# Optimization experiments

Measured on AMD Instinct MI355X. Metric: run time of the kernel, lower is better.

## Reference

```python
import jax, jax.numpy as jnp
import numpy as np

SIMOTA_Q = 10
W_CLS, W_GEOM, W_IOU, W_DIST, W_THETA = 4.0, 5.0, 2.0, 1.0, 2.0
INVALID = -100000.0
LINE_HALF_WIDTH = 15.0


def _pairwise_line_iou(pred_xs, gt_xs):
    # pred_xs [B,N,S], gt_xs [B,M,S] -> iou [B,N,M] (CLRNet-style line IoU)
    p = pred_xs[:, :, None, :]  # [B,N,1,S]
    t = gt_xs[:, None, :, :]    # [B,1,M,S]
    inv = (p == INVALID) | (t == INVALID)
    ovr = jnp.minimum(p + LINE_HALF_WIDTH, t + LINE_HALF_WIDTH) - jnp.maximum(p - LINE_HALF_WIDTH, t - LINE_HALF_WIDTH)
    union = jnp.maximum(p + LINE_HALF_WIDTH, t + LINE_HALF_WIDTH) - jnp.minimum(p - LINE_HALF_WIDTH, t - LINE_HALF_WIDTH)
    ovr = jnp.where(inv, 0.0, ovr)
    union = jnp.where(inv, 0.0, union)
    return ovr.sum(-1) / (union.sum(-1) + 1e-9)


def setup_inputs() -> dict:
    key = jax.random.key(0)
    ks = jax.random.split(key, 12)
    B, N, M, S = 16, 1000, 24, 72
    img_w, img_h = 800, 320
    # preds: [logit0, logit1, start_y, start_x, theta(deg), length, delta_x*S]
    p = jnp.concatenate([
        jax.random.normal(ks[0], (B, N, 2)),
        jax.random.uniform(ks[1], (B, N, 1), minval=img_h * 0.4, maxval=img_h - 1.0),
        jax.random.uniform(ks[2], (B, N, 1), minval=0.0, maxval=img_w - 1.0),
        jax.random.uniform(ks[3], (B, N, 1), minval=20.0, maxval=160.0),
        jax.random.uniform(ks[4], (B, N, 1), minval=10.0, maxval=float(img_h)),
        jax.random.normal(ks[5], (B, N, S)) * 5.0,
    ], axis=-1)
    t = jnp.concatenate([
        jnp.zeros((B, M, 2)),
        jax.random.uniform(ks[6], (B, M, 1), minval=img_h * 0.5, maxval=img_h - 1.0),
        jax.random.uniform(ks[7], (B, M, 1), minval=50.0, maxval=img_w - 50.0),
        jax.random.uniform(ks[8], (B, M, 1), minval=30.0, maxval=150.0),
        jax.random.uniform(ks[9], (B, M, 1), minval=10.0, maxval=float(img_h)),
        jax.random.normal(ks[10], (B, M, S)) * 5.0,
    ], axis=-1)
    masks = jax.random.bernoulli(ks[11], 0.5, (B, M))
    return {"preds": p.astype(jnp.float32), "targets": t.astype(jnp.float32),
            "masks": masks, "img_w": img_w, "img_h": img_h}


def reference(preds, targets, masks, img_w, img_h):
    B, N, C = preds.shape
    M = targets.shape[1]
    S = C - 6
    dt = preds.dtype
    sample_ys = jnp.linspace(img_h - 1.0, 0.0, S, dtype=dt).reshape(1, 1, S)

    p_sy, p_sx, p_th, p_len = preds[..., 2], preds[..., 3], preds[..., 4], preds[..., 5]
    p_dx = preds[..., 6:]
    g_sy, g_sx, g_th = targets[..., 2], targets[..., 3], targets[..., 4]
    g_dx = targets[..., 6:]

    # absolute sample-x for preds and gts along row anchors
    p_tan = jnp.clip(jnp.tan(jnp.deg2rad(p_th)), -1000.0, 1000.0)
    p_xs = p_sx[..., None] + (p_sy[..., None] - sample_ys) * p_tan[..., None] + p_dx  # [B,N,S]
    g_tan = jnp.clip(jnp.tan(jnp.deg2rad(g_th)), -1000.0, 1000.0)
    g_xs = g_sx[..., None] + (g_sy[..., None] - sample_ys) * g_tan[..., None] + g_dx  # [B,M,S]

    p_valid = (sample_ys >= (p_sy - p_len)[..., None]) & (sample_ys <= p_sy[..., None])
    p_xs = jnp.where(p_valid, p_xs, INVALID)
    g_inv = (g_dx < -10000.0) | (g_xs < 0) | (g_xs >= img_w)
    g_xs = jnp.where(g_inv, INVALID, g_xs)

    ious = jnp.nan_to_num(_pairwise_line_iou(p_xs, g_xs), nan=0.0)  # [B,N,M]
    ious = jnp.where(masks[:, None, :], ious, 0.0)
    iou_cost = 1.0 - ious

    dx = (p_sx[:, :, None] - g_sx[:, None, :]) / (img_w - 1)
    dy = (p_sy[:, :, None] - g_sy[:, None, :]) / (img_h - 1)
    dist_cost = jnp.sqrt(dx * dx + dy * dy + 1e-8)
    theta_cost = jnp.abs((p_th[:, :, None] - g_th[:, None, :]) / 90.0)
    geom_cost = W_DIST * dist_cost + W_THETA * theta_cost

    score = jax.nn.softmax(preds[..., :2], axis=-1)[..., 1]
    cls_cost = -jnp.log(jnp.clip(score, 1e-8))[:, :, None]

    total = W_CLS * cls_cost + W_GEOM * geom_cost + W_IOU * iou_cost
    total = jnp.where(masks[:, None, :], total, 100000.0)

    # dynamic-k: since dynamic_ks <= SIMOTA_Q always, use fixed K (extra slots masked by k_mask)
    K = min(SIMOTA_Q, N)
    topk_ious, _ = jax.lax.top_k(jnp.swapaxes(ious, 1, 2), K)       # [B,M,K]
    dynamic_ks = jnp.clip(topk_ious.sum(-1).astype(jnp.int32), 1, N)  # [B,M]
    _, topk_idx = jax.lax.top_k(-jnp.swapaxes(total, 1, 2), K)      # smallest costs, [B,M,K]
    topk_idx = jnp.swapaxes(topk_idx, 1, 2)                         # [B,K,M]
    k_mask = jnp.arange(K)[None, :, None] < dynamic_ks[:, None, :]  # [B,K,M]

    b_ix = jnp.arange(B)[:, None, None]
    m_ix = jnp.arange(M)[None, None, :]
    matching = jnp.zeros((B, N, M), dt).at[b_ix, topk_idx, m_ix].set(k_mask.astype(dt))
    matching = jnp.where(masks[:, None, :], matching, 0.0)

    # conflict resolution: anchors matched to >1 gt keep only min-cost gt
    conflict = matching.sum(-1) > 1.0
    cost_inf = jnp.where(matching == 0.0, jnp.inf, total)
    min_idx = jnp.argmin(cost_inf, axis=2)
    matching = jnp.where(conflict[..., None], jax.nn.one_hot(min_idx, M, dtype=dt), matching)

    assigned = matching.sum(-1) > 0
    matched = jnp.argmax(matching, axis=2)
    matched = jnp.where(assigned, matched, -1)
    return assigned, matched
```

## Files before the change

### kernel.cpp

```cpp
#include <hip/hip_runtime.h>
#include <math.h>
#include <float.h>

#define Bb 16
#define Nn 1000
#define NP 1024
#define Mm 24
#define Ss 72
#define Cc 78
#define Kk 10
#define NCH 4
#define INVALIDF (-100000.0f)
#define DEG2RAD 0.017453292519943295f

struct Hdr { int mask_mode; int pad0; int pad1; int pad2; };

#define CHSZ       (Bb*Mm*NCH*Kk*4)
#define OFF_CHTOT  16
#define OFF_CHIDX  (OFF_CHTOT + CHSZ)
#define OFF_CHIOU  (OFF_CHIDX + CHSZ)
#define OFF_PMETA  ((OFF_CHIOU + CHSZ + 255) & ~255)
#define OFF_PXS    (OFF_PMETA + Bb*NP*16)
#define WS6_NEEDED (OFF_PXS + Bb*Ss*NP*4)

__device__ __forceinline__ float read_dim(const void* p) {
    int v = *(const int*)p;
    if (v <= 0 || v > 1000000) v = (int)(*(const float*)p);
    return (float)v;
}

__device__ __forceinline__ bool mask_at(const void* m, int mode, int idx) {
    if (mode == 0) return ((const unsigned char*)m)[idx] != 0;
    if (mode == 1) return ((const int*)m)[idx] != 0;
    return ((const float*)m)[idx] != 0.0f;
}

__device__ __forceinline__ void bitonic64(float& v, int& i, const int lane) {
#pragma unroll
    for (int k = 2; k <= 64; k <<= 1) {
#pragma unroll
        for (int j = k >> 1; j >= 1; j >>= 1) {
            const float pv = __shfl_xor(v, j, 64);
            const int   pi = __shfl_xor(i, j, 64);
            const bool keepMin = (((lane & k) == 0) == ((lane & j) == 0));
            const bool meLess  = (v < pv) || (v == pv && i < pi);
            if (keepMin ? !meLess : meLess) { v = pv; i = pi; }
        }
    }
}

__global__ __launch_bounds__(256) void k_prep(
    const float* __restrict__ preds, const unsigned char* __restrict__ mb,
    const void* __restrict__ hp,
    Hdr* __restrict__ hdr, float* __restrict__ pxs, float4* __restrict__ pmeta)
{
    __shared__ float lds[32 * Cc];
    __shared__ float ys[Ss];
    __shared__ float ssx[32], ssy[32], sptan[32], slo[32];
    __shared__ int s_nz, s_f32;

    const int tid = threadIdx.x;
    const int base = blockIdx.x * 32;

    const float4* src4 = (const float4*)(preds + (size_t)base * Cc);
    float4* lds4 = (float4*)lds;
    for (int i = tid; i < (32 * Cc) / 4; i += 256) lds4[i] = src4[i];

    const float ih = read_dim(hp);
    if (tid < Ss)
        ys[tid] = (float)((double)(ih - 1.0f) * (double)(Ss - 1 - tid) / (double)(Ss - 1));

    if (blockIdx.x == 0) {
        if (tid == 0) { s_nz = 0; s_f32 = 0; }
        __syncthreads();
        if (tid < (Bb * Mm) / 4) {
            const uchar4 c4 = *(const uchar4*)(mb + tid * 4);
            int nz = (c4.y ? 1 : 0) + (c4.z ? 1 : 0) + (c4.w ? 1 : 0);
            bool f = (c4.x == 0x80 || c4.x == 0x3f) || (c4.y == 0x80 || c4.y == 0x3f) ||
                     (c4.z == 0x80 || c4.z == 0x3f) || (c4.w == 0x80 || c4.w == 0x3f);
            if (nz) atomicAdd(&s_nz, nz);
            if (f)  atomicOr(&s_f32, 1);
        }
        __syncthreads();
        if (tid == 0)
            hdr->mask_mode = (s_nz == 0) ? 1 : (s_f32 ? 2 : 0);
    }
    __syncthreads();

    if (tid < 32) {
        const float* pr = lds + tid * Cc;
        const float p0 = pr[0], p1 = pr[1];
        const float sy = pr[2], sx = pr[3], th = pr[4], len = pr[5];
        const float mx = fmaxf(p0, p1);
        const float e0 = expf(p0 - mx), e1 = expf(p1 - mx);
        float score = fmaxf(e1 / (e0 + e1), 1e-8f);
        const float cls = -logf(score);
        ssx[tid] = sx; ssy[tid] = sy;
        sptan[tid] = fminf(fmaxf(tanf(th * DEG2RAD), -1000.0f), 1000.0f);
        slo[tid] = sy - len;

        const int p = base + tid;
        const int b = p / Nn, n = p - b * Nn;
        pmeta[(b << 10) | n] = make_float4(cls, sx, sy, th);
    }
    __syncthreads();

    const int nn = tid & 31, srow = tid >> 5;
    const int p = base + nn;
    const int b = p / Nn, n = p - b * Nn;
    const float sx = ssx[nn], sy = ssy[nn], ptan = sptan[nn], lo = slo[nn];
    const float* dxr = lds + nn * Cc + 6;
    for (int s = srow; s < Ss; s += 8) {
        const float y = ys[s];
        const float px = sx + (sy - y) * ptan + dxr[s];
        const bool valid = (y >= lo) && (y <= sy);
        pxs[(((size_t)b * Ss + s) << 10) | n] = valid ? px : INVALIDF;
    }
}

__global__ __launch_bounds__(256) void k_colE(
    const float* __restrict__ targs, const void* __restrict__ masks,
    const Hdr* __restrict__ hdr, const float* __restrict__ pxs,
    const float4* __restrict__ pmeta, const void* __restrict__ wp,
    const void* __restrict__ hp,
    float* __restrict__ chtot, int* __restrict__ chidx, float* __restrict__ chiou)
{
    __shared__ float gx[Ss];
    __shared__ float wtot[4][Kk];
    __shared__ int   widx[4][Kk];
    __shared__ float wiou[4][Kk];

    const int col   = blockIdx.x >> 2;
    const int chunk = blockIdx.x & 3;
    const int b     = col / Mm;
    const int tid   = threadIdx.x;

    if (!mask_at(masks, hdr->mask_mode, col)) return;

    const float iw = read_dim(wp);
    const float ih = read_dim(hp);
    const float* tg = targs + (size_t)col * Cc;
    const float g_sy = tg[2], g_sx = tg[3], g_th = tg[4];
    const float g_tan = fminf(fmaxf(tanf(g_th * DEG2RAD), -1000.0f), 1000.0f);

    if (tid < Ss) {
        const float y = (float)((double)(ih - 1.0f) * (double)(Ss - 1 - tid) / (double)(Ss - 1));
        const float gdx = tg[6 + tid];
        float v = g_sx + (g_sy - y) * g_tan + gdx;
        if (gdx < -10000.0f || v < 0.0f || v >= iw) v = INVALIDF;
        gx[tid] = v;
    }
    __syncthreads();

    const int n = chunk * 256 + tid;
    float ov = 0.0f, un = 0.0f;
    const float* pxb = pxs + (((size_t)b * Ss) << 10);
#pragma unroll 8
    for (int s = 0; s < Ss; ++s) {
        const float g = gx[s];
        const float px = pxb[(s << 10) | n];
        if (g != INVALIDF && px != INVALIDF) {
            const float d = fabsf(px - g);
            ov += 30.0f - d;
            un += 30.0f + d;
        }
    }

    const float4 me = pmeta[(b << 10) + n];
    const float iouv = ov / (un + 1e-9f);
    const float dxn = (me.y - g_sx) / (iw - 1.0f);
    const float dyn = (me.z - g_sy) / (ih - 1.0f);
    const float dist = sqrtf(dxn * dxn + dyn * dyn + 1e-8f);
    const float theta = fabsf((me.w - g_th) / 90.0f);
    const float geom = 1.0f * dist + 2.0f * theta;
    const float t = 4.0f * me.x + 5.0f * geom + 2.0f * (1.0f - iouv);

    const int w = tid >> 6, lane = tid & 63;

    float v1 = (n < Nn) ? t : FLT_MAX;     int i1 = n;
    bitonic64(v1, i1, lane);
    if (lane < Kk) { wtot[w][lane] = v1; widx[w][lane] = i1; }

    float v2 = (n < Nn) ? -iouv : FLT_MAX; int i2 = n;
    bitonic64(v2, i2, lane);
    if (lane < Kk) wiou[w][lane] = v2;
    __syncthreads();

    const int obase = blockIdx.x * Kk;
    if (w == 0) {
        float v = FLT_MAX; int i = 0x7fffffff;
        if (lane < NCH * Kk) { v = wtot[lane / Kk][lane % Kk]; i = widx[lane / Kk][lane % Kk]; }
        bitonic64(v, i, lane);
        if (lane < Kk) { chtot[obase + lane] = v; chidx[obase + lane] = i; }
    } else if (w == 1) {
        float v = FLT_MAX; int i = lane;
        if (lane < NCH * Kk) v = wiou[lane / Kk][lane % Kk];
        bitonic64(v, i, lane);
        if (lane < Kk) chiou[obase + lane] = -v;
    }
}

__global__ __launch_bounds__(1024) void k_final(
    const void* __restrict__ masks, const Hdr* __restrict__ hdr,
    const float* __restrict__ chtot, const int* __restrict__ chidx,
    const float* __restrict__ chiou, int* __restrict__ out)
{
    __shared__ float stot[Mm * NCH * Kk];
    __shared__ int   sidx[Mm * NCH * Kk];
    __shared__ float siou[Mm * NCH * Kk];
    __shared__ int   s_sel[Mm * Kk];
    __shared__ float s_tot[Mm * Kk];
    __shared__ int   s_dk[Mm];
    __shared__ int   maskok[Mm];

    const int b   = blockIdx.x;
    const int tid = threadIdx.x;
    const int mode = hdr->mask_mode;

    const int bbase = b * (Mm * NCH * Kk);
    if (tid < Mm * NCH * Kk) {
        stot[tid] = chtot[bbase + tid];
        sidx[tid] = chidx[bbase + tid];
        siou[tid] = chiou[bbase + tid];
    }
    if (tid < Mm) maskok[tid] = mask_at(masks, mode, b * Mm + tid) ? 1 : 0;
    __syncthreads();

    const int w = tid >> 6, lane = tid & 63;
    for (int m = w; m < Mm; m += 16) {
        if (!maskok[m]) {
            if (lane == 0) s_dk[m] = 0;
            continue;
        }
        float v = FLT_MAX; int i = 0x7fffffff;
        if (lane < NCH * Kk) { v = stot[m * NCH * Kk + lane]; i = sidx[m * NCH * Kk + lane]; }
        bitonic64(v, i, lane);
        if (lane < Kk) { s_sel[m * Kk + lane] = i; s_tot[m * Kk + lane] = v; }

        float v2 = FLT_MAX; int i2 = lane;
        if (lane < NCH * Kk) v2 = -siou[m * NCH * Kk + lane];
        bitonic64(v2, i2, lane);
        float isum = 0.0f;
#pragma unroll
        for (int k = 0; k < Kk; ++k) isum += -__shfl(v2, k, 64);
        if (lane == 0) {
            int dk = (int)isum;
            dk = (dk < 1) ? 1 : (dk > Kk ? Kk : dk);
            s_dk[m] = dk;
        }
    }
    __syncthreads();

    if (tid < Nn) {
        const int n = tid;
        int cnt = 0, firstm = -1, bestm = -1;
        float bestv = FLT_MAX;
        for (int m = 0; m < Mm; ++m) {
            const int dk = s_dk[m];
            for (int k = 0; k < dk; ++k) {
                if (s_sel[m * Kk + k] == n) {
                    const float tv = s_tot[m * Kk + k];
                    cnt++;
                    if (firstm < 0) firstm = m;
                    if (tv < bestv) { bestv = tv; bestm = m; }
                    break;
                }
            }
        }
        int matched;
        if (cnt == 0)      matched = -1;
        else if (cnt == 1) matched = firstm;
        else               matched = bestm;

        const int gid = b * Nn + n;
        out[gid]           = (cnt > 0) ? 1 : 0;
        out[Bb * Nn + gid] = matched;
    }
}

#define OFF_FSELK   16
#define OFF_FSELTOT (OFF_FSELK + Bb*Mm*Kk*4)
#define OFF_FDYNK   (OFF_FSELTOT + Bb*Mm*Kk*4)

__global__ void k_detect_fb(const unsigned char* __restrict__ mb, Hdr* __restrict__ hdr) {
    int nz_off = 0; bool f32pat = false;
    for (int i = 0; i < Bb * Mm; ++i) {
        unsigned char c = mb[i];
        if ((i & 3) && c) nz_off++;
        if (c == 0x80 || c == 0x3f) f32pat = true;
    }
    hdr->mask_mode = (nz_off == 0) ? 1 : (f32pat ? 2 : 0);
}

__global__ __launch_bounds__(256) void k_col_fb(
    const float* __restrict__ preds, const float* __restrict__ targs,
    const void* __restrict__ masks, const Hdr* __restrict__ hdr,
    const void* __restrict__ wp, const void* __restrict__ hp,
    int* __restrict__ selk, float* __restrict__ seltot, int* __restrict__ dynk)
{
    __shared__ float ys[Ss];
    __shared__ float gx[Ss];
    __shared__ float iou_s[Nn];
    __shared__ float tot_s[Nn];
    __shared__ float rv[256];
    __shared__ int   ri[256];

    const int bm = blockIdx.x;
    const int b  = bm / Mm;
    const int tid = threadIdx.x;
    const float iw = read_dim(wp);
    const float ih = read_dim(hp);

    if (!mask_at(masks, hdr->mask_mode, bm)) {
        if (tid == 0) dynk[bm] = 0;
        return;
    }
    if (tid < Ss)
        ys[tid] = (float)((double)(ih - 1.0f) * (double)(Ss - 1 - tid) / (double)(Ss - 1));
    __syncthreads();

    const float* tg = targs + (size_t)bm * Cc;
    const float g_sy = tg[2], g_sx = tg[3], g_th = tg[4];
    const float g_tan = fminf(fmaxf(tanf(g_th * DEG2RAD), -1000.0f), 1000.0f);
    if (tid < Ss) {
        float gdx = tg[6 + tid];
        float v = g_sx + (g_sy - ys[tid]) * g_tan + gdx;
        if (gdx < -10000.0f || v < 0.0f || v >= iw) v = INVALIDF;
        gx[tid] = v;
    }
    __syncthreads();

    for (int n = tid; n < Nn; n += 256) {
        const float* pr = preds + ((size_t)b * Nn + n) * Cc;
        const float p0 = pr[0], p1 = pr[1];
        const float sy = pr[2], sx = pr[3], th = pr[4], len = pr[5];
        const float mx = fmaxf(p0, p1);
        const float e0 = expf(p0 - mx), e1 = expf(p1 - mx);
        float score = fmaxf(e1 / (e0 + e1), 1e-8f);
        const float cls = -logf(score);
        const float ptan = fminf(fmaxf(tanf(th * DEG2RAD), -1000.0f), 1000.0f);
        const float lo = sy - len;
        float ov = 0.0f, un = 0.0f;
        for (int s = 0; s < Ss; ++s) {
            const float y = ys[s];
            const float t = gx[s];
            if (y >= lo && y <= sy && t != INVALIDF) {
                const float px = sx + (sy - y) * ptan + pr[6 + s];
                if (px != INVALIDF) {
                    const float d = fabsf(px - t);
                    ov += 30.0f - d;
                    un += 30.0f + d;
                }
            }
        }
        const float iou = ov / (un + 1e-9f);
        const float dxn = (sx - g_sx) / (iw - 1.0f);
        const float dyn = (sy - g_sy) / (ih - 1.0f);
        const float dist = sqrtf(dxn * dxn + dyn * dyn + 1e-8f);
        const float theta = fabsf((th - g_th) / 90.0f);
        const float tot = 4.0f * cls + 5.0f * (1.0f * dist + 2.0f * theta) + 2.0f * (1.0f - iou);
        iou_s[n] = iou;
        tot_s[n] = tot;
    }
    __syncthreads();

    for (int k = 0; k < Kk; ++k) {
        float bv = FLT_MAX; int bi = 0x7fffffff;
        for (int n = tid; n < Nn; n += 256) {
            const float v = tot_s[n];
            if (v < bv) { bv = v; bi = n; }
        }
        rv[tid] = bv; ri[tid] = bi;
        __syncthreads();
        for (int off = 128; off > 0; off >>= 1) {
            if (tid < off) {
                const float v2 = rv[tid + off]; const int i2 = ri[tid + off];
                if (v2 < rv[tid] || (v2 == rv[tid] && i2 < ri[tid])) { rv[tid] = v2; ri[tid] = i2; }
            }
            __syncthreads();
        }
        if (tid == 0) {
            const int c = ri[0];
            selk[bm * Kk + k] = c;
            seltot[bm * Kk + k] = tot_s[c];
            tot_s[c] = FLT_MAX;
        }
        __syncthreads();
    }

    float isum = 0.0f;
    for (int k = 0; k < Kk; ++k) {
        float bv = -FLT_MAX; int bi = 0x7fffffff;
        for (int n = tid; n < Nn; n += 256) {
            const float v = iou_s[n];
            if (v > bv) { bv = v; bi = n; }
        }
        rv[tid] = bv; ri[tid] = bi;
        __syncthreads();
        for (int off = 128; off > 0; off >>= 1) {
            if (tid < off) {
                const float v2 = rv[tid + off]; const int i2 = ri[tid + off];
                if (v2 > rv[tid] || (v2 == rv[tid] && i2 < ri[tid])) { rv[tid] = v2; ri[tid] = i2; }
            }
            __syncthreads();
        }
        if (tid == 0) {
            const int c = ri[0];
            isum += iou_s[c];
            iou_s[c] = -FLT_MAX;
        }
        __syncthreads();
    }
    if (tid == 0) {
        int dk = (int)isum;
        dk = (dk < 1) ? 1 : (dk > Nn ? Nn : dk);
        dynk[bm] = dk;
    }
}

__global__ __launch_bounds__(256) void k_resolve_fb(
    const int* __restrict__ selk, const float* __restrict__ seltot,
    const int* __restrict__ dynk, int* __restrict__ out)
{
    const int gid = blockIdx.x * 256 + threadIdx.x;
    if (gid >= Bb * Nn) return;
    const int b = gid / Nn;
    const int n = gid % Nn;

    int cnt = 0, firstm = -1, bestm = -1;
    float bestv = FLT_MAX;
    for (int m = 0; m < Mm; ++m) {
        const int bm = b * Mm + m;
        const int dk = dynk[bm];
        for (int k = 0; k < dk && k < Kk; ++k) {
            if (selk[bm * Kk + k] == n) {
                const float tv = seltot[bm * Kk + k];
                cnt++;
                if (firstm < 0) firstm = m;
                if (tv < bestv) { bestv = tv; bestm = m; }
                break;
            }
        }
    }
    int matched;
    if (cnt == 0)      matched = -1;
    else if (cnt == 1) matched = firstm;
    else               matched = bestm;

    out[gid]           = (cnt > 0) ? 1 : 0;
    out[Bb * Nn + gid] = matched;
}

extern "C" void kernel_launch(void* const* d_in, const int* in_sizes, int n_in,
                              void* d_out, int out_size, void* d_ws, size_t ws_size,
                              hipStream_t stream) {
    const float* preds = (const float*)d_in[0];
    const float* targs = (const float*)d_in[1];
    const void*  masks = d_in[2];
    const void*  wp    = d_in[3];
    const void*  hp    = d_in[4];
    int* out = (int*)d_out;

    char* ws = (char*)d_ws;
    Hdr* hdr = (Hdr*)ws;

    if (ws_size >= (size_t)WS6_NEEDED) {
        float*  chtot = (float*)(ws + OFF_CHTOT);
        int*    chidx = (int*)(ws + OFF_CHIDX);
        float*  chiou = (float*)(ws + OFF_CHIOU);
        float4* pmeta = (float4*)(ws + OFF_PMETA);
        float*  pxs   = (float*)(ws + OFF_PXS);

        k_prep<<<Bb * Nn / 32, 256, 0, stream>>>(preds, (const unsigned char*)masks, hp,
                                                 hdr, pxs, pmeta);
        k_colE<<<Bb * Mm * NCH, 256, 0, stream>>>(targs, masks, hdr, pxs, pmeta,
                                                  wp, hp, chtot, chidx, chiou);
        k_final<<<Bb, 1024, 0, stream>>>(masks, hdr, chtot, chidx, chiou, out);
    } else {
        int*   selk   = (int*)(ws + OFF_FSELK);
        float* seltot = (float*)(ws + OFF_FSELTOT);
        int*   dynk   = (int*)(ws + OFF_FDYNK);
        k_detect_fb<<<1, 1, 0, stream>>>((const unsigned char*)masks, hdr);
        k_col_fb<<<Bb * Mm, 256, 0, stream>>>(preds, targs, masks, hdr, wp, hp,
                                              selk, seltot, dynk);
        k_resolve_fb<<<(Bb * Nn + 255) / 256, 256, 0, stream>>>(selk, seltot, dynk, out);
    }
}
```

Before: 46.48 us.

## Fuse final assignment into column kernel via last-block atomic counter

Removes the separate k_final launch. Each column block now bumps a per-batch atomic counter, and the last of its 96 blocks performs the per-batch merge and conflict resolution in place. The counter is reset in the prep kernel. Both kernels also remap block indices so that a batch's blocks spread across XCDs, which is meant to improve locality and balance, and prep now uses per-batch 32-row tiles with a partial tail. This saves one launch and its gap, but the final stage now runs serially on a single 256-thread block per batch and depends on threadfence/atomic ordering.

```diff
diff --git a/kernel.cpp b/kernel.cpp
--- a/kernel.cpp
+++ b/kernel.cpp
@@ -15,13 +15,14 @@
 
 struct Hdr { int mask_mode; int pad0; int pad1; int pad2; };
 
+#define OFF_CNT    16
+#define OFF_CHTOT  128
 #define CHSZ       (Bb*Mm*NCH*Kk*4)
-#define OFF_CHTOT  16
 #define OFF_CHIDX  (OFF_CHTOT + CHSZ)
 #define OFF_CHIOU  (OFF_CHIDX + CHSZ)
 #define OFF_PMETA  ((OFF_CHIOU + CHSZ + 255) & ~255)
 #define OFF_PXS    (OFF_PMETA + Bb*NP*16)
-#define WS6_NEEDED (OFF_PXS + Bb*Ss*NP*4)
+#define WS7_NEEDED (OFF_PXS + Bb*Ss*NP*4)
 
 __device__ __forceinline__ float read_dim(const void* p) {
     int v = *(const int*)p;
@@ -49,10 +50,11 @@
     }
 }
 
-__global__ __launch_bounds__(256) void k_prep(
+__global__ __launch_bounds__(256) void k_prep2(
     const float* __restrict__ preds, const unsigned char* __restrict__ mb,
     const void* __restrict__ hp,
-    Hdr* __restrict__ hdr, float* __restrict__ pxs, float4* __restrict__ pmeta)
+    Hdr* __restrict__ hdr, int* __restrict__ cnt,
+    float* __restrict__ pxs, float4* __restrict__ pmeta)
 {
     __shared__ float lds[32 * Cc];
     __shared__ float ys[Ss];
@@ -60,17 +62,23 @@
     __shared__ int s_nz, s_f32;
 
     const int tid = threadIdx.x;
-    const int base = blockIdx.x * 32;
-
-    const float4* src4 = (const float4*)(preds + (size_t)base * Cc);
+    const int q = blockIdx.x;
+    const int L = ((q & 7) << 6) | (q >> 3);
+    const int b   = L >> 5;
+    const int blk = L & 31;
+    const int base_n = blk * 32;
+    const int valid = (base_n + 32 <= Nn) ? 32 : (Nn - base_n);
+
+    const float4* src4 = (const float4*)(preds + ((size_t)b * Nn + base_n) * Cc);
     float4* lds4 = (float4*)lds;
-    for (int i = tid; i < (32 * Cc) / 4; i += 256) lds4[i] = src4[i];
+    const int n4 = (valid * Cc) / 4;
+    for (int i = tid; i < n4; i += 256) lds4[i] = src4[i];
 
     const float ih = read_dim(hp);
     if (tid < Ss)
         ys[tid] = (float)((double)(ih - 1.0f) * (double)(Ss - 1 - tid) / (double)(Ss - 1));
 
-    if (blockIdx.x == 0) {
+    if (q == 0) {
         if (tid == 0) { s_nz = 0; s_f32 = 0; }
         __syncthreads();
         if (tid < (Bb * Mm) / 4) {
@@ -84,10 +92,11 @@
         __syncthreads();
         if (tid == 0)
             hdr->mask_mode = (s_nz == 0) ? 1 : (s_f32 ? 2 : 0);
-    }
-    __syncthreads();
-
-    if (tid < 32) {
+        if (tid < Bb) cnt[tid] = 0;
+    }
+    __syncthreads();
+
+    if (tid < valid) {
         const float* pr = lds + tid * Cc;
         const float p0 = pr[0], p1 = pr[1];
         const float sy = pr[2], sx = pr[3], th = pr[4], len = pr[5];
@@ -98,147 +107,149 @@
         ssx[tid] = sx; ssy[tid] = sy;
         sptan[tid] = fminf(fmaxf(tanf(th * DEG2RAD), -1000.0f), 1000.0f);
         slo[tid] = sy - len;
-
-        const int p = base + tid;
-        const int b = p / Nn, n = p - b * Nn;
-        pmeta[(b << 10) | n] = make_float4(cls, sx, sy, th);
+        pmeta[(b << 10) | (base_n + tid)] = make_float4(cls, sx, sy, th);
     }
     __syncthreads();
 
     const int nn = tid & 31, srow = tid >> 5;
-    const int p = base + nn;
-    const int b = p / Nn, n = p - b * Nn;
-    const float sx = ssx[nn], sy = ssy[nn], ptan = sptan[nn], lo = slo[nn];
-    const float* dxr = lds + nn * Cc + 6;
-    for (int s = srow; s < Ss; s += 8) {
-        const float y = ys[s];
-        const float px = sx + (sy - y) * ptan + dxr[s];
-        const bool valid = (y >= lo) && (y <= sy);
-        pxs[(((size_t)b * Ss + s) << 10) | n] = valid ? px : INVALIDF;
-    }
-}
-
-__global__ __launch_bounds__(256) void k_colE(
+    if (nn < valid) {
+        const int n = base_n + nn;
+        const float sx = ssx[nn], sy = ssy[nn], ptan = sptan[nn], lo = slo[nn];
+        const float* dxr = lds + nn * Cc + 6;
+        for (int s = srow; s < Ss; s += 8) {
+            const float y = ys[s];
+            const float px = sx + (sy - y) * ptan + dxr[s];
+            const bool valid_s = (y >= lo) && (y <= sy);
+            pxs[(((size_t)b * Ss + s) << 10) | n] = valid_s ? px : INVALIDF;
+        }
+    }
+}
+
+__global__ __launch_bounds__(256) void k_colF(
     const float* __restrict__ targs, const void* __restrict__ masks,
     const Hdr* __restrict__ hdr, const float* __restrict__ pxs,
     const float4* __restrict__ pmeta, const void* __restrict__ wp,
-    const void* __restrict__ hp,
-    float* __restrict__ chtot, int* __restrict__ chidx, float* __restrict__ chiou)
+    const void* __restrict__ hp, int* __restrict__ cnt,
+    float* __restrict__ chtot, int* __restrict__ chidx, float* __restrict__ chiou,
+    int* __restrict__ out)
 {
     __shared__ float gx[Ss];
     __shared__ float wtot[4][Kk];
     __shared__ int   widx[4][Kk];
     __shared__ float wiou[4][Kk];
-
-    const int col   = blockIdx.x >> 2;
-    const int chunk = blockIdx.x & 3;
-    const int b     = col / Mm;
-    const int tid   = threadIdx.x;
-
-    if (!mask_at(masks, hdr->mask_mode, col)) return;
-
-    const float iw = read_dim(wp);
-    const float ih = read_dim(hp);
-    const float* tg = targs + (size_t)col * Cc;
-    const float g_sy = tg[2], g_sx = tg[3], g_th = tg[4];
-    const float g_tan = fminf(fmaxf(tanf(g_th * DEG2RAD), -1000.0f), 1000.0f);
-
-    if (tid < Ss) {
-        const float y = (float)((double)(ih - 1.0f) * (double)(Ss - 1 - tid) / (double)(Ss - 1));
-        const float gdx = tg[6 + tid];
-        float v = g_sx + (g_sy - y) * g_tan + gdx;
-        if (gdx < -10000.0f || v < 0.0f || v >= iw) v = INVALIDF;
-        gx[tid] = v;
-    }
-    __syncthreads();
-
-    const int n = chunk * 256 + tid;
-    float ov = 0.0f, un = 0.0f;
-    const float* pxb = pxs + (((size_t)b * Ss) << 10);
-#pragma unroll 8
-    for (int s = 0; s < Ss; ++s) {
-        const float g = gx[s];
-        const float px = pxb[(s << 10) | n];
-        if (g != INVALIDF && px != INVALIDF) {
-            const float d = fabsf(px - g);
-            ov += 30.0f - d;
-            un += 30.0f + d;
-        }
-    }
-
-    const float4 me = pmeta[(b << 10) + n];
-    const float iouv = ov / (un + 1e-9f);
-    const float dxn = (me.y - g_sx) / (iw - 1.0f);
-    const float dyn = (me.z - g_sy) / (ih - 1.0f);
-    const float dist = sqrtf(dxn * dxn + dyn * dyn + 1e-8f);
-    const float theta = fabsf((me.w - g_th) / 90.0f);
-    const float geom = 1.0f * dist + 2.0f * theta;
-    const float t = 4.0f * me.x + 5.0f * geom + 2.0f * (1.0f - iouv);
-
-    const int w = tid >> 6, lane = tid & 63;
-
-    float v1 = (n < Nn) ? t : FLT_MAX;     int i1 = n;
-    bitonic64(v1, i1, lane);
-    if (lane < Kk) { wtot[w][lane] = v1; widx[w][lane] = i1; }
-
-    float v2 = (n < Nn) ? -iouv : FLT_MAX; int i2 = n;
-    bitonic64(v2, i2, lane);
-    if (lane < Kk) wiou[w][lane] = v2;
-    __syncthreads();
-
-    const int obase = blockIdx.x * Kk;
-    if (w == 0) {
-        float v = FLT_MAX; int i = 0x7fffffff;
-        if (lane < NCH * Kk) { v = wtot[lane / Kk][lane % Kk]; i = widx[lane / Kk][lane % Kk]; }
-        bitonic64(v, i, lane);
-        if (lane < Kk) { chtot[obase + lane] = v; chidx[obase + lane] = i; }
-    } else if (w == 1) {
-        float v = FLT_MAX; int i = lane;
-        if (lane < NCH * Kk) v = wiou[lane / Kk][lane % Kk];
-        bitonic64(v, i, lane);
-        if (lane < Kk) chiou[obase + lane] = -v;
-    }
-}
-
-__global__ __launch_bounds__(1024) void k_final(
-    const void* __restrict__ masks, const Hdr* __restrict__ hdr,
-    const float* __restrict__ chtot, const int* __restrict__ chidx,
-    const float* __restrict__ chiou, int* __restrict__ out)
-{
+    __shared__ int   s_last;
     __shared__ float stot[Mm * NCH * Kk];
     __shared__ int   sidx[Mm * NCH * Kk];
     __shared__ float siou[Mm * NCH * Kk];
     __shared__ int   s_sel[Mm * Kk];
     __shared__ float s_tot[Mm * Kk];
     __shared__ int   s_dk[Mm];
-    __shared__ int   maskok[Mm];
-
-    const int b   = blockIdx.x;
+
+    const int P = blockIdx.x;
+    const int L = (P & 7) * 192 + (P >> 3);
+    const int b = L / 96;
+    const int r = L - b * 96;
+    const int m = r >> 2;
+    const int chunk = r & 3;
+    const int col = b * Mm + m;
     const int tid = threadIdx.x;
     const int mode = hdr->mask_mode;
 
+    const float iw = read_dim(wp);
+    const float ih = read_dim(hp);
+
+    if (mask_at(masks, mode, col)) {
+        const float* tg = targs + (size_t)col * Cc;
+        const float g_sy = tg[2], g_sx = tg[3], g_th = tg[4];
+        const float g_tan = fminf(fmaxf(tanf(g_th * DEG2RAD), -1000.0f), 1000.0f);
+
+        if (tid < Ss) {
+            const float y = (float)((double)(ih - 1.0f) * (double)(Ss - 1 - tid) / (double)(Ss - 1));
+            const float gdx = tg[6 + tid];
+            float v = g_sx + (g_sy - y) * g_tan + gdx;
+            if (gdx < -10000.0f || v < 0.0f || v >= iw) v = INVALIDF;
+            gx[tid] = v;
+        }
+        __syncthreads();
+
+        const int n = chunk * 256 + tid;
+        float ov = 0.0f, un = 0.0f;
+        const float* pxb = pxs + (((size_t)b * Ss) << 10);
+#pragma unroll 8
+        for (int s = 0; s < Ss; ++s) {
+            const float g = gx[s];
+            const float px = pxb[(s << 10) | n];
+            if (g != INVALIDF && px != INVALIDF) {
+                const float d = fabsf(px - g);
+                ov += 30.0f - d;
+                un += 30.0f + d;
+            }
+        }
+
+        const float4 me = pmeta[(b << 10) + n];
+        const float iouv = ov / (un + 1e-9f);
+        const float dxn = (me.y - g_sx) / (iw - 1.0f);
+        const float dyn = (me.z - g_sy) / (ih - 1.0f);
+        const float dist = sqrtf(dxn * dxn + dyn * dyn + 1e-8f);
+        const float theta = fabsf((me.w - g_th) / 90.0f);
+        const float geom = 1.0f * dist + 2.0f * theta;
+        const float t = 4.0f * me.x + 5.0f * geom + 2.0f * (1.0f - iouv);
+
+        const int w = tid >> 6, lane = tid & 63;
+
+        float v1 = (n < Nn) ? t : FLT_MAX;     int i1 = n;
+        bitonic64(v1, i1, lane);
+        if (lane < Kk) { wtot[w][lane] = v1; widx[w][lane] = i1; }
+
+        float v2 = (n < Nn) ? -iouv : FLT_MAX; int i2 = n;
+        bitonic64(v2, i2, lane);
+        if (lane < Kk) wiou[w][lane] = v2;
+        __syncthreads();
+
+        const int obase = L * Kk;
+        if (w == 0) {
+            float v = FLT_MAX; int i = 0x7fffffff;
+            if (lane < NCH * Kk) { v = wtot[lane / Kk][lane % Kk]; i = widx[lane / Kk][lane % Kk]; }
+            bitonic64(v, i, lane);
+            if (lane < Kk) { chtot[obase + lane] = v; chidx[obase + lane] = i; }
+        } else if (w == 1) {
+            float v = FLT_MAX; int i = lane;
+            if (lane < NCH * Kk) v = wiou[lane / Kk][lane % Kk];
+            bitonic64(v, i, lane);
+            if (lane < Kk) chiou[obase + lane] = -v;
+        }
+    }
+
+    __threadfence();
+    if (tid == 0) {
+        const int done = atomicAdd(&cnt[b], 1);
+        s_last = (done == 95) ? 1 : 0;
+    }
+    __syncthreads();
+    if (!s_last) return;
+    __threadfence();
+
     const int bbase = b * (Mm * NCH * Kk);
-    if (tid < Mm * NCH * Kk) {
-        stot[tid] = chtot[bbase + tid];
-        sidx[tid] = chidx[bbase + tid];
-        siou[tid] = chiou[bbase + tid];
-    }
-    if (tid < Mm) maskok[tid] = mask_at(masks, mode, b * Mm + tid) ? 1 : 0;
+    for (int i = tid; i < Mm * NCH * Kk; i += 256) {
+        stot[i] = chtot[bbase + i];
+        sidx[i] = chidx[bbase + i];
+        siou[i] = chiou[bbase + i];
+    }
     __syncthreads();
 
     const int w = tid >> 6, lane = tid & 63;
-    for (int m = w; m < Mm; m += 16) {
-        if (!maskok[m]) {
-            if (lane == 0) s_dk[m] = 0;
+    for (int mm = w; mm < Mm; mm += 4) {
+        if (!mask_at(masks, mode, b * Mm + mm)) {
+            if (lane == 0) s_dk[mm] = 0;
             continue;
         }
         float v = FLT_MAX; int i = 0x7fffffff;
-        if (lane < NCH * Kk) { v = stot[m * NCH * Kk + lane]; i = sidx[m * NCH * Kk + lane]; }
+        if (lane < NCH * Kk) { v = stot[mm * NCH * Kk + lane]; i = sidx[mm * NCH * Kk + lane]; }
         bitonic64(v, i, lane);
-        if (lane < Kk) { s_sel[m * Kk + lane] = i; s_tot[m * Kk + lane] = v; }
+        if (lane < Kk) { s_sel[mm * Kk + lane] = i; s_tot[mm * Kk + lane] = v; }
 
         float v2 = FLT_MAX; int i2 = lane;
-        if (lane < NCH * Kk) v2 = -siou[m * NCH * Kk + lane];
+        if (lane < NCH * Kk) v2 = -siou[mm * NCH * Kk + lane];
         bitonic64(v2, i2, lane);
         float isum = 0.0f;
 #pragma unroll
@@ -246,34 +257,33 @@
         if (lane == 0) {
             int dk = (int)isum;
             dk = (dk < 1) ? 1 : (dk > Kk ? Kk : dk);
-            s_dk[m] = dk;
-        }
-    }
-    __syncthreads();
-
-    if (tid < Nn) {
-        const int n = tid;
-        int cnt = 0, firstm = -1, bestm = -1;
+            s_dk[mm] = dk;
+        }
+    }
+    __syncthreads();
+
+    for (int n = tid; n < Nn; n += 256) {
+        int cnt2 = 0, firstm = -1, bestm = -1;
         float bestv = FLT_MAX;
-        for (int m = 0; m < Mm; ++m) {
-            const int dk = s_dk[m];
+        for (int mm = 0; mm < Mm; ++mm) {
+            const int dk = s_dk[mm];
             for (int k = 0; k < dk; ++k) {
-                if (s_sel[m * Kk + k] == n) {
-                    const float tv = s_tot[m * Kk + k];
-                    cnt++;
-                    if (firstm < 0) firstm = m;
-                    if (tv < bestv) { bestv = tv; bestm = m; }
+                if (s_sel[mm * Kk + k] == n) {
+                    const float tv = s_tot[mm * Kk + k];
+                    cnt2++;
+                    if (firstm < 0) firstm = mm;
+                    if (tv < bestv) { bestv = tv; bestm = mm; }
                     break;
                 }
             }
         }
         int matched;
-        if (cnt == 0)      matched = -1;
-        else if (cnt == 1) matched = firstm;
-        else               matched = bestm;
+        if (cnt2 == 0)      matched = -1;
+        else if (cnt2 == 1) matched = firstm;
+        else                matched = bestm;
 
         const int gid = b * Nn + n;
-        out[gid]           = (cnt > 0) ? 1 : 0;
+        out[gid]           = (cnt2 > 0) ? 1 : 0;
         out[Bb * Nn + gid] = matched;
     }
 }
@@ -464,18 +474,18 @@
     char* ws = (char*)d_ws;
     Hdr* hdr = (Hdr*)ws;
 
-    if (ws_size >= (size_t)WS6_NEEDED) {
+    if (ws_size >= (size_t)WS7_NEEDED) {
+        int*    cnt   = (int*)(ws + OFF_CNT);
         float*  chtot = (float*)(ws + OFF_CHTOT);
         int*    chidx = (int*)(ws + OFF_CHIDX);
         float*  chiou = (float*)(ws + OFF_CHIOU);
         float4* pmeta = (float4*)(ws + OFF_PMETA);
         float*  pxs   = (float*)(ws + OFF_PXS);
 
-        k_prep<<<Bb * Nn / 32, 256, 0, stream>>>(preds, (const unsigned char*)masks, hp,
-                                                 hdr, pxs, pmeta);
-        k_colE<<<Bb * Mm * NCH, 256, 0, stream>>>(targs, masks, hdr, pxs, pmeta,
-                                                  wp, hp, chtot, chidx, chiou);
-        k_final<<<Bb, 1024, 0, stream>>>(masks, hdr, chtot, chidx, chiou, out);
+        k_prep2<<<512, 256, 0, stream>>>(preds, (const unsigned char*)masks, hp,
+                                         hdr, cnt, pxs, pmeta);
+        k_colF<<<Bb * Mm * NCH, 256, 0, stream>>>(targs, masks, hdr, pxs, pmeta,
+                                                  wp, hp, cnt, chtot, chidx, chiou, out);
     } else {
         int*   selk   = (int*)(ws + OFF_FSELK);
         float* seltot = (float*)(ws + OFF_FSELTOT);
```

After: 148.2 us. +218.9%, slower.

## Process six GT columns per block to reuse each prediction-point load

Applied to the files above, without the earlier changes.

The column kernel now handles a group of six ground-truth lanes per block instead of one. Each block loads every prediction x-coordinate once and accumulates overlap/union for all six targets in registers. The grid shrinks from one block per (column, chunk) to one per (batch, chunk, group of six), cutting redundant global reads of the prediction coordinate buffer. In exchange there are far fewer blocks (256) to fill the GPU, more registers per thread, and serialized per-column bitonic sorts inside each block.

```diff
diff --git a/kernel.cpp b/kernel.cpp
--- a/kernel.cpp
+++ b/kernel.cpp
@@ -10,6 +10,7 @@
 #define Cc 78
 #define Kk 10
 #define NCH 4
+#define CPG 6
 #define INVALIDF (-100000.0f)
 #define DEG2RAD 0.017453292519943295f
 
@@ -118,85 +119,116 @@
     }
 }
 
-__global__ __launch_bounds__(256) void k_colE(
+__global__ __launch_bounds__(256) void k_colG(
     const float* __restrict__ targs, const void* __restrict__ masks,
     const Hdr* __restrict__ hdr, const float* __restrict__ pxs,
     const float4* __restrict__ pmeta, const void* __restrict__ wp,
     const void* __restrict__ hp,
     float* __restrict__ chtot, int* __restrict__ chidx, float* __restrict__ chiou)
 {
-    __shared__ float gx[Ss];
-    __shared__ float wtot[4][Kk];
-    __shared__ int   widx[4][Kk];
-    __shared__ float wiou[4][Kk];
-
-    const int col   = blockIdx.x >> 2;
-    const int chunk = blockIdx.x & 3;
-    const int b     = col / Mm;
+    __shared__ float gxs[CPG][Ss];
+    __shared__ float gsx[CPG], gsy[CPG], gth[CPG], gtan[CPG];
+    __shared__ int   maskok[CPG];
+    __shared__ float wtot[CPG][4][Kk];
+    __shared__ int   widx[CPG][4][Kk];
+    __shared__ float wiou[CPG][4][Kk];
+
+    const int bid   = blockIdx.x;
+    const int b     = bid >> 4;
+    const int chunk = (bid >> 2) & 3;
+    const int mg    = bid & 3;
+    const int m0    = mg * CPG;
     const int tid   = threadIdx.x;
-
-    if (!mask_at(masks, hdr->mask_mode, col)) return;
+    const int mode  = hdr->mask_mode;
 
     const float iw = read_dim(wp);
     const float ih = read_dim(hp);
-    const float* tg = targs + (size_t)col * Cc;
-    const float g_sy = tg[2], g_sx = tg[3], g_th = tg[4];
-    const float g_tan = fminf(fmaxf(tanf(g_th * DEG2RAD), -1000.0f), 1000.0f);
-
-    if (tid < Ss) {
-        const float y = (float)((double)(ih - 1.0f) * (double)(Ss - 1 - tid) / (double)(Ss - 1));
-        const float gdx = tg[6 + tid];
-        float v = g_sx + (g_sy - y) * g_tan + gdx;
+
+    if (tid < CPG) {
+        const int col = b * Mm + m0 + tid;
+        maskok[tid] = mask_at(masks, mode, col) ? 1 : 0;
+        const float* tg = targs + (size_t)col * Cc;
+        gsy[tid] = tg[2]; gsx[tid] = tg[3]; gth[tid] = tg[4];
+        gtan[tid] = fminf(fmaxf(tanf(tg[4] * DEG2RAD), -1000.0f), 1000.0f);
+    }
+    __syncthreads();
+
+    for (int e = tid; e < CPG * Ss; e += 256) {
+        const int j = e / Ss, s = e - j * Ss;
+        const int col = b * Mm + m0 + j;
+        const float y = (float)((double)(ih - 1.0f) * (double)(Ss - 1 - s) / (double)(Ss - 1));
+        const float gdx = targs[(size_t)col * Cc + 6 + s];
+        float v = gsx[j] + (gsy[j] - y) * gtan[j] + gdx;
         if (gdx < -10000.0f || v < 0.0f || v >= iw) v = INVALIDF;
-        gx[tid] = v;
+        gxs[j][s] = v;
     }
     __syncthreads();
 
     const int n = chunk * 256 + tid;
-    float ov = 0.0f, un = 0.0f;
+    float ov[CPG] = {0.f, 0.f, 0.f, 0.f, 0.f, 0.f};
+    float un[CPG] = {0.f, 0.f, 0.f, 0.f, 0.f, 0.f};
     const float* pxb = pxs + (((size_t)b * Ss) << 10);
-#pragma unroll 8
+#pragma unroll 4
     for (int s = 0; s < Ss; ++s) {
-        const float g = gx[s];
         const float px = pxb[(s << 10) | n];
-        if (g != INVALIDF && px != INVALIDF) {
-            const float d = fabsf(px - g);
-            ov += 30.0f - d;
-            un += 30.0f + d;
+#pragma unroll
+        for (int j = 0; j < CPG; ++j) {
+            const float g = gxs[j][s];
+            if (g != INVALIDF && px != INVALIDF) {
+                const float d = fabsf(px - g);
+                ov[j] += 30.0f - d;
+                un[j] += 30.0f + d;
+            }
         }
     }
 
     const float4 me = pmeta[(b << 10) + n];
-    const float iouv = ov / (un + 1e-9f);
-    const float dxn = (me.y - g_sx) / (iw - 1.0f);
-    const float dyn = (me.z - g_sy) / (ih - 1.0f);
-    const float dist = sqrtf(dxn * dxn + dyn * dyn + 1e-8f);
-    const float theta = fabsf((me.w - g_th) / 90.0f);
-    const float geom = 1.0f * dist + 2.0f * theta;
-    const float t = 4.0f * me.x + 5.0f * geom + 2.0f * (1.0f - iouv);
-
     const int w = tid >> 6, lane = tid & 63;
 
-    float v1 = (n < Nn) ? t : FLT_MAX;     int i1 = n;
-    bitonic64(v1, i1, lane);
-    if (lane < Kk) { wtot[w][lane] = v1; widx[w][lane] = i1; }
-
-    float v2 = (n < Nn) ? -iouv : FLT_MAX; int i2 = n;
-    bitonic64(v2, i2, lane);
-    if (lane < Kk) wiou[w][lane] = v2;
-    __syncthreads();
-
-    const int obase = blockIdx.x * Kk;
-    if (w == 0) {
-        float v = FLT_MAX; int i = 0x7fffffff;
-        if (lane < NCH * Kk) { v = wtot[lane / Kk][lane % Kk]; i = widx[lane / Kk][lane % Kk]; }
-        bitonic64(v, i, lane);
-        if (lane < Kk) { chtot[obase + lane] = v; chidx[obase + lane] = i; }
-    } else if (w == 1) {
-        float v = FLT_MAX; int i = lane;
-        if (lane < NCH * Kk) v = wiou[lane / Kk][lane % Kk];
-        bitonic64(v, i, lane);
-        if (lane < Kk) chiou[obase + lane] = -v;
+    float tot[CPG], iou[CPG];
+#pragma unroll
+    for (int j = 0; j < CPG; ++j) {
+        const float iouv = ov[j] / (un[j] + 1e-9f);
+        const float dxn = (me.y - gsx[j]) / (iw - 1.0f);
+        const float dyn = (me.z - gsy[j]) / (ih - 1.0f);
+        const float dist = sqrtf(dxn * dxn + dyn * dyn + 1e-8f);
+        const float theta = fabsf((me.w - gth[j]) / 90.0f);
+        const float geom = 1.0f * dist + 2.0f * theta;
+        const float t = 4.0f * me.x + 5.0f * geom + 2.0f * (1.0f - iouv);
+        tot[j] = (n < Nn) ? t : FLT_MAX;
+        iou[j] = (n < Nn) ? iouv : -FLT_MAX;
+    }
+
+#pragma unroll
+    for (int j = 0; j < CPG; ++j) {
+        if (maskok[j]) {
+            float v1 = tot[j]; int i1 = n;
+            bitonic64(v1, i1, lane);
+            if (lane < Kk) { wtot[j][w][lane] = v1; widx[j][w][lane] = i1; }
+
+            float v2 = -iou[j]; int i2 = n;
+            bitonic64(v2, i2, lane);
+            if (lane < Kk) wiou[j][w][lane] = v2;
+        }
+    }
+    __syncthreads();
+
+    for (int task = w; task < 2 * CPG; task += 4) {
+        const int j = task >> 1;
+        if (!maskok[j]) continue;
+        const int col = b * Mm + m0 + j;
+        const int obase = (col * NCH + chunk) * Kk;
+        if ((task & 1) == 0) {
+            float v = FLT_MAX; int i = 0x7fffffff;
+            if (lane < 4 * Kk) { v = wtot[j][lane / Kk][lane % Kk]; i = widx[j][lane / Kk][lane % Kk]; }
+            bitonic64(v, i, lane);
+            if (lane < Kk) { chtot[obase + lane] = v; chidx[obase + lane] = i; }
+        } else {
+            float v = FLT_MAX; int i = lane;
+            if (lane < 4 * Kk) v = wiou[j][lane / Kk][lane % Kk];
+            bitonic64(v, i, lane);
+            if (lane < Kk) chiou[obase + lane] = -v;
+        }
     }
 }
 
@@ -473,8 +505,8 @@
 
         k_prep<<<Bb * Nn / 32, 256, 0, stream>>>(preds, (const unsigned char*)masks, hp,
                                                  hdr, pxs, pmeta);
-        k_colE<<<Bb * Mm * NCH, 256, 0, stream>>>(targs, masks, hdr, pxs, pmeta,
-                                                  wp, hp, chtot, chidx, chiou);
+        k_colG<<<Bb * NCH * 4, 256, 0, stream>>>(targs, masks, hdr, pxs, pmeta,
+                                                 wp, hp, chtot, chidx, chiou);
         k_final<<<Bb, 1024, 0, stream>>>(masks, hdr, chtot, chidx, chiou, out);
     } else {
         int*   selk   = (int*)(ws + OFF_FSELK);
```

New measurement: 96.72 us. 2.08x slower.
